# Kernel tuning notes

Measured on AMD Instinct MI355X. Metric: run time of the kernel, lower is better.

Reference implementation:

```python
import jax, jax.numpy as jnp
import numpy as np

EPS = 1e-12  # torch F.normalize default eps

def _l2norm(x):
    n = jnp.linalg.norm(x, axis=-1, keepdims=True)
    return x / jnp.maximum(n, EPS)

def setup_inputs() -> dict:
    key = jax.random.key(0)
    k1, k2, k3, k4 = jax.random.split(key, 4)
    B, D = 8192, 768           # batch, emb_d
    P, L = 4096, 8             # e_pool_size, e_p_length
    x_querry = jax.random.normal(k1, (B, D), dtype=jnp.float32)
    x_block = jax.random.normal(k2, (B, D), dtype=jnp.float32)
    # tensor_prompt uses nn.init.uniform_ -> U[0,1)
    e_k = jax.random.uniform(k3, (P, D), dtype=jnp.float32)
    e_p = jax.random.uniform(k4, (P, L, D), dtype=jnp.float32)
    return {"x_querry": x_querry, "x_block": x_block, "e_k": e_k, "e_p": e_p, "l": 3}

def reference(x_querry, x_block, e_k, e_p, l):
    # DualAdapt.forward with l=3 (e-layer), train=False: cosine-sim routing + gather
    assert l in (3, 4, 5), "reference covers the e-layer (prompt routing) path"
    n_K = _l2norm(e_k)                                  # [P, D]
    q = jax.lax.stop_gradient(_l2norm(x_querry))        # [B, D] (q is .detach()'d)
    cos_sim = jnp.einsum('bj,kj->bk', q, n_K)           # [B, P]
    k_idx = jnp.argmax(cos_sim, axis=1)                 # top_k = 1 -> indices[:, 0]
    P_ = e_p[k_idx]                                     # gather: [B, L, D]
    i = e_p.shape[1] // 2                               # e_p_length / 2
    Ek = P_[:, :i, :]                                   # [B, L/2, D]
    Ev = P_[:, i:, :]                                   # [B, L/2, D]
    # eval path: loss = 0, x_block untouched for e-layers
    return (Ek, Ev, x_block)
```

## Files before the change

kernel.cpp:

```cpp
#include <hip/hip_runtime.h>
#include <math.h>

#define NQ   8192
#define NK   4096
#define DIM  768
#define LL   8

typedef _Float16 f16;
typedef __attribute__((ext_vector_type(4))) _Float16 f16x4;
typedef __attribute__((ext_vector_type(8))) _Float16 f16x8;
typedef __attribute__((ext_vector_type(4))) float f32x4;
typedef unsigned long long u64;

__device__ inline unsigned ordf(float f) {
    unsigned u = __float_as_uint(f);
    return (u & 0x80000000u) ? ~u : (u | 0x80000000u);
}

__device__ __forceinline__ void gload16(const void* g, void* l) {
    __builtin_amdgcn_global_load_lds((const __attribute__((address_space(1))) void*)g,
                                     (__attribute__((address_space(3))) void*)l, 16, 0, 0);
}

__global__ __launch_bounds__(256) void prep(const float* __restrict__ xq,
                                            const float* __restrict__ ek,
                                            f16* __restrict__ Xh,
                                            f16* __restrict__ Eh,
                                            float* __restrict__ margin,
                                            float* __restrict__ inv_n) {
    const int wid = threadIdx.x >> 6, lane = threadIdx.x & 63;
    const int row = blockIdx.x * 4 + wid;
    const bool isX = row < NQ;
    const f32x4* src = (const f32x4*)(isX ? xq + (size_t)row * DIM
                                          : ek + (size_t)(row - NQ) * DIM);
    f16x4* dst = (f16x4*)(isX ? Xh + (size_t)row * DIM : Eh + (size_t)(row - NQ) * DIM);
    float s2 = 0.f;
#pragma unroll
    for (int j = 0; j < 3; ++j) {
        const f32x4 v = src[j * 64 + lane];
        s2 = fmaf(v.x, v.x, fmaf(v.y, v.y, fmaf(v.z, v.z, fmaf(v.w, v.w, s2))));
        dst[j * 64 + lane] = (f16x4){(f16)v.x, (f16)v.y, (f16)v.z, (f16)v.w};
    }
#pragma unroll
    for (int off = 32; off; off >>= 1) s2 += __shfl_xor(s2, off);
    if (lane == 0) {
        if (isX) margin[row] = sqrtf(s2) * 1.5e-4f + 2e-3f;
        else     inv_n[row - NQ] = 1.0f / fmaxf(sqrtf(s2), 1e-12f);
    }
}

__global__ __launch_bounds__(256) void gemm97(const f16* __restrict__ Xh,
                                              const f16* __restrict__ Eh,
                                              const float* __restrict__ inv_n,
                                              f16* __restrict__ scor) {
    __shared__ f16 A[128 * 64], B[128 * 64];
    const int t = threadIdx.x, lane = t & 63, wid = t >> 6;
    const int wm = wid & 1, wn = wid >> 1;
    const int qbase = blockIdx.x * 128, kbase = blockIdx.y * 128;

    f32x4 acc[4][4];
#pragma unroll
    for (int mi = 0; mi < 4; ++mi)
#pragma unroll
        for (int ni = 0; ni < 4; ++ni) acc[mi][ni] = (f32x4){0.f, 0.f, 0.f, 0.f};

    const int srow = wid * 8 + (lane >> 3);
    const int scol = (lane & 7) * 8;
    const f16* gA = Xh + (size_t)(qbase + srow) * DIM + scol;
    const f16* gB = Eh + (size_t)(kbase + srow) * DIM + scol;
    f16* lA = &A[wid * 512 + lane * 8];
    f16* lB = &B[wid * 512 + lane * 8];

    for (int kk = 0; kk < DIM; kk += 64) {
        __syncthreads();
#pragma unroll
        for (int p = 0; p < 4; ++p) {
            gload16(gA + (size_t)(p * 32) * DIM + kk, lA + p * 2048);
            gload16(gB + (size_t)(p * 32) * DIM + kk, lB + p * 2048);
        }
        __syncthreads();

#pragma unroll
        for (int kk2 = 0; kk2 < 2; ++kk2) {
            const int ko = kk2 * 32 + (lane >> 4) * 8;
            f16x8 ah[4], bh[4];
#pragma unroll
            for (int mi = 0; mi < 4; ++mi)
                ah[mi] = *(const f16x8*)&A[(wm * 64 + mi * 16 + (lane & 15)) * 64 + ko];
#pragma unroll
            for (int ni = 0; ni < 4; ++ni)
                bh[ni] = *(const f16x8*)&B[(wn * 64 + ni * 16 + (lane & 15)) * 64 + ko];
#pragma unroll
            for (int mi = 0; mi < 4; ++mi)
#pragma unroll
                for (int ni = 0; ni < 4; ++ni)
                    acc[mi][ni] = __builtin_amdgcn_mfma_f32_16x16x32_f16(ah[mi], bh[ni], acc[mi][ni], 0, 0, 0);
        }
    }

    const int rg = lane >> 4, cid = lane & 15;
    float invv[4];
    int key[4];
#pragma unroll
    for (int ni = 0; ni < 4; ++ni) {
        key[ni] = kbase + wn * 64 + ni * 16 + cid;
        invv[ni] = inv_n[key[ni]];
    }
#pragma unroll
    for (int mi = 0; mi < 4; ++mi)
#pragma unroll
        for (int rj = 0; rj < 4; ++rj) {
            const int row = qbase + wm * 64 + mi * 16 + rg * 4 + rj;
#pragma unroll
            for (int ni = 0; ni < 4; ++ni)
                scor[(size_t)row * NK + key[ni]] = (f16)(acc[mi][ni][rj] * invv[ni]);
        }
}

__global__ __launch_bounds__(256) void scan_rescore(const f16* __restrict__ scor,
                                                    const float* __restrict__ margin,
                                                    const float* __restrict__ inv_n,
                                                    const float* __restrict__ xq,
                                                    const float* __restrict__ ek,
                                                    int* __restrict__ bestk) {
    const int r = blockIdx.x, t = threadIdx.x, lane = t & 63, wid = t >> 6;
    __shared__ float wmaxs[4];
    __shared__ u64 wbest[4];
    __shared__ int cnt;
    __shared__ int list[256];

    if (t == 0) cnt = 0;

    const f16* srow = scor + (size_t)r * NK + t * 16;
    const f16x8 s0 = *(const f16x8*)srow;
    const f16x8 s1 = *(const f16x8*)(srow + 8);
    float sc[16];
    float m = -INFINITY;
#pragma unroll
    for (int j = 0; j < 8; ++j) { sc[j] = (float)s0[j]; sc[j + 8] = (float)s1[j]; }
#pragma unroll
    for (int j = 0; j < 16; ++j) m = fmaxf(m, sc[j]);
#pragma unroll
    for (int off = 32; off; off >>= 1) m = fmaxf(m, __shfl_xor(m, off));
    if (lane == 0) wmaxs[wid] = m;
    __syncthreads();
    m = fmaxf(fmaxf(wmaxs[0], wmaxs[1]), fmaxf(wmaxs[2], wmaxs[3]));
    const float thr = m - margin[r];

#pragma unroll
    for (int j = 0; j < 16; ++j) {
        if (sc[j] >= thr) {
            const int idx = atomicAdd(&cnt, 1);
            if (idx < 256) list[idx] = t * 16 + j;
        }
    }
    __syncthreads();
    const int n = cnt < 256 ? cnt : 256;

    const f32x4* xr = (const f32x4*)(xq + (size_t)r * DIM);
    const f32x4 xa = xr[lane * 3], xb = xr[lane * 3 + 1], xc = xr[lane * 3 + 2];

    u64 best = 0;
    for (int e = wid; e < n; e += 4) {
        const int k = list[e];
        const f32x4* er = (const f32x4*)(ek + (size_t)k * DIM);
        const f32x4 ea = er[lane * 3], eb = er[lane * 3 + 1], ec = er[lane * 3 + 2];
        float s = xa.x * ea.x;
        s = fmaf(xa.y, ea.y, s); s = fmaf(xa.z, ea.z, s); s = fmaf(xa.w, ea.w, s);
        s = fmaf(xb.x, eb.x, s); s = fmaf(xb.y, eb.y, s); s = fmaf(xb.z, eb.z, s);
        s = fmaf(xb.w, eb.w, s); s = fmaf(xc.x, ec.x, s); s = fmaf(xc.y, ec.y, s);
        s = fmaf(xc.z, ec.z, s); s = fmaf(xc.w, ec.w, s);
#pragma unroll
        for (int off = 32; off; off >>= 1) s += __shfl_xor(s, off);
        const float v = s * inv_n[k];
        const u64 p64 = ((u64)ordf(v) << 32) | (unsigned)(NK - 1 - k);
        best = best > p64 ? best : p64;
    }
    if (lane == 0) wbest[wid] = best;
    __syncthreads();
    if (t == 0) {
        u64 b0 = wbest[0];
        b0 = b0 > wbest[1] ? b0 : wbest[1];
        b0 = b0 > wbest[2] ? b0 : wbest[2];
        b0 = b0 > wbest[3] ? b0 : wbest[3];
        bestk[r] = NK - 1 - (int)(unsigned)(b0 & 0xffffffffu);
    }
}

__global__ __launch_bounds__(256) void gather_flat(const int* __restrict__ bestk,
                                                   const float* __restrict__ e_p,
                                                   const float* __restrict__ x_block,
                                                   f32x4* __restrict__ o) {
    const int EK4 = NQ * 4 * (DIM / 4);
    const int XB4 = 2 * EK4;
    const int TOT = XB4 + NQ * (DIM / 4);
    const int stride = gridDim.x * 256;
    const f32x4* ep4 = (const f32x4*)e_p;
    const f32x4* xb4 = (const f32x4*)x_block;
#pragma unroll 1
    for (int f = blockIdx.x * 256 + threadIdx.x; f < TOT; f += stride) {
        f32x4 v;
        if (f < XB4) {
            const int g = (f >= EK4) ? f - EK4 : f;
            const int b = g / (4 * DIM / 4);
            const int k = bestk[b];
            const int off = (f >= EK4) ? 4 * (DIM / 4) : 0;
            v = ep4[(size_t)k * (LL * DIM / 4) + off + (g - b * 768)];
        } else {
            v = __builtin_nontemporal_load(&xb4[f - XB4]);
        }
        __builtin_nontemporal_store(v, &o[f]);
    }
}

extern "C" void kernel_launch(void* const* d_in, const int* in_sizes, int n_in,
                              void* d_out, int out_size, void* d_ws, size_t ws_size,
                              hipStream_t stream) {
    const float* x_querry = (const float*)d_in[0];
    const float* x_block  = (const float*)d_in[1];
    const float* e_k      = (const float*)d_in[2];
    const float* e_p      = (const float*)d_in[3];

    char* base = (char*)d_out;
    f16*   Xh   = (f16*)(base);
    f16*   Eh   = (f16*)(base + 12582912);
    float* invn = (float*)(base + 18874368);
    float* marg = (float*)(base + 18890752);
    f16*   scor = (f16*)(base + 18923520);
    int*   bestk = (int*)d_ws;

    prep<<<(NQ + NK) / 4, 256, 0, stream>>>(x_querry, e_k, Xh, Eh, marg, invn);
    gemm97<<<dim3(NQ / 128, NK / 128), 256, 0, stream>>>(Xh, Eh, invn, scor);
    scan_rescore<<<NQ, 256, 0, stream>>>(scor, marg, invn, x_querry, e_k, bestk);
    gather_flat<<<2048, 256, 0, stream>>>(bestk, e_p, x_block, (f32x4*)d_out);
}
```

Baseline: 175.8 us.

## Fuse candidate filtering into GEMM epilogue, drop score matrix, enlarge tiles

```diff
diff --git a/kernel.cpp b/kernel.cpp
--- a/kernel.cpp
+++ b/kernel.cpp
@@ -5,6 +5,7 @@
 #define NK   4096
 #define DIM  768
 #define LL   8
+#define CCAP 64
 
 typedef _Float16 f16;
 typedef __attribute__((ext_vector_type(4))) _Float16 f16x4;
@@ -15,6 +16,10 @@
 __device__ inline unsigned ordf(float f) {
     unsigned u = __float_as_uint(f);
     return (u & 0x80000000u) ? ~u : (u | 0x80000000u);
+}
+__device__ inline float iord(unsigned u) {
+    unsigned b = (u & 0x80000000u) ? (u & 0x7fffffffu) : ~u;
+    return __uint_as_float(b);
 }
 
 __device__ __forceinline__ void gload16(const void* g, void* l) {
@@ -49,49 +54,50 @@
     }
 }
 
-__global__ __launch_bounds__(256) void gemm97(const f16* __restrict__ Xh,
-                                              const f16* __restrict__ Eh,
-                                              const float* __restrict__ inv_n,
-                                              f16* __restrict__ scor) {
-    __shared__ f16 A[128 * 64], B[128 * 64];
+__global__ __launch_bounds__(512, 2) void gemm256(const f16* __restrict__ Xh,
+                                                  const f16* __restrict__ Eh,
+                                                  const float* __restrict__ inv_n,
+                                                  const float* __restrict__ marg,
+                                                  int* __restrict__ cnt,
+                                                  u64* __restrict__ cand) {
+    __shared__ f16 A[256 * 64], B[256 * 64];
+    __shared__ float rmax[4][256];
     const int t = threadIdx.x, lane = t & 63, wid = t >> 6;
     const int wm = wid & 1, wn = wid >> 1;
-    const int qbase = blockIdx.x * 128, kbase = blockIdx.y * 128;
-
-    f32x4 acc[4][4];
-#pragma unroll
-    for (int mi = 0; mi < 4; ++mi)
+    const int qbase = blockIdx.x * 256, kbase = blockIdx.y * 256;
+
+    f32x4 acc[8][4];
+#pragma unroll
+    for (int mi = 0; mi < 8; ++mi)
 #pragma unroll
         for (int ni = 0; ni < 4; ++ni) acc[mi][ni] = (f32x4){0.f, 0.f, 0.f, 0.f};
 
-    const int srow = wid * 8 + (lane >> 3);
-    const int scol = (lane & 7) * 8;
-    const f16* gA = Xh + (size_t)(qbase + srow) * DIM + scol;
-    const f16* gB = Eh + (size_t)(kbase + srow) * DIM + scol;
-    f16* lA = &A[wid * 512 + lane * 8];
-    f16* lB = &B[wid * 512 + lane * 8];
+    const f16* gA = Xh + (size_t)(qbase + (t >> 3)) * DIM + (t & 7) * 8;
+    const f16* gB = Eh + (size_t)(kbase + (t >> 3)) * DIM + (t & 7) * 8;
+    f16* lA = &A[t * 8];
+    f16* lB = &B[t * 8];
 
     for (int kk = 0; kk < DIM; kk += 64) {
         __syncthreads();
 #pragma unroll
         for (int p = 0; p < 4; ++p) {
-            gload16(gA + (size_t)(p * 32) * DIM + kk, lA + p * 2048);
-            gload16(gB + (size_t)(p * 32) * DIM + kk, lB + p * 2048);
+            gload16(gA + (size_t)(p * 64) * DIM + kk, lA + p * 4096);
+            gload16(gB + (size_t)(p * 64) * DIM + kk, lB + p * 4096);
         }
         __syncthreads();
 
 #pragma unroll
         for (int kk2 = 0; kk2 < 2; ++kk2) {
             const int ko = kk2 * 32 + (lane >> 4) * 8;
-            f16x8 ah[4], bh[4];
-#pragma unroll
-            for (int mi = 0; mi < 4; ++mi)
-                ah[mi] = *(const f16x8*)&A[(wm * 64 + mi * 16 + (lane & 15)) * 64 + ko];
+            f16x8 ah[8], bh[4];
+#pragma unroll
+            for (int mi = 0; mi < 8; ++mi)
+                ah[mi] = *(const f16x8*)&A[(wm * 128 + mi * 16 + (lane & 15)) * 64 + ko];
 #pragma unroll
             for (int ni = 0; ni < 4; ++ni)
                 bh[ni] = *(const f16x8*)&B[(wn * 64 + ni * 16 + (lane & 15)) * 64 + ko];
 #pragma unroll
-            for (int mi = 0; mi < 4; ++mi)
+            for (int mi = 0; mi < 8; ++mi)
 #pragma unroll
                 for (int ni = 0; ni < 4; ++ni)
                     acc[mi][ni] = __builtin_amdgcn_mfma_f32_16x16x32_f16(ah[mi], bh[ni], acc[mi][ni], 0, 0, 0);
@@ -106,63 +112,73 @@
         key[ni] = kbase + wn * 64 + ni * 16 + cid;
         invv[ni] = inv_n[key[ni]];
     }
-#pragma unroll
-    for (int mi = 0; mi < 4; ++mi)
+
+#pragma unroll
+    for (int mi = 0; mi < 8; ++mi)
 #pragma unroll
         for (int rj = 0; rj < 4; ++rj) {
-            const int row = qbase + wm * 64 + mi * 16 + rg * 4 + rj;
-#pragma unroll
-            for (int ni = 0; ni < 4; ++ni)
-                scor[(size_t)row * NK + key[ni]] = (f16)(acc[mi][ni][rj] * invv[ni]);
-        }
-}
-
-__global__ __launch_bounds__(256) void scan_rescore(const f16* __restrict__ scor,
-                                                    const float* __restrict__ margin,
-                                                    const float* __restrict__ inv_n,
-                                                    const float* __restrict__ xq,
-                                                    const float* __restrict__ ek,
-                                                    int* __restrict__ bestk) {
-    const int r = blockIdx.x, t = threadIdx.x, lane = t & 63, wid = t >> 6;
-    __shared__ float wmaxs[4];
-    __shared__ u64 wbest[4];
-    __shared__ int cnt;
-    __shared__ int list[256];
-
-    if (t == 0) cnt = 0;
-
-    const f16* srow = scor + (size_t)r * NK + t * 16;
-    const f16x8 s0 = *(const f16x8*)srow;
-    const f16x8 s1 = *(const f16x8*)(srow + 8);
-    float sc[16];
-    float m = -INFINITY;
-#pragma unroll
-    for (int j = 0; j < 8; ++j) { sc[j] = (float)s0[j]; sc[j + 8] = (float)s1[j]; }
-#pragma unroll
-    for (int j = 0; j < 16; ++j) m = fmaxf(m, sc[j]);
-#pragma unroll
-    for (int off = 32; off; off >>= 1) m = fmaxf(m, __shfl_xor(m, off));
-    if (lane == 0) wmaxs[wid] = m;
+            float lm = acc[mi][0][rj] * invv[0];
+            lm = fmaxf(lm, acc[mi][1][rj] * invv[1]);
+            lm = fmaxf(lm, acc[mi][2][rj] * invv[2]);
+            lm = fmaxf(lm, acc[mi][3][rj] * invv[3]);
+#pragma unroll
+            for (int off = 1; off < 16; off <<= 1) lm = fmaxf(lm, __shfl_xor(lm, off));
+            if (cid == 0) rmax[wn][wm * 128 + mi * 16 + rg * 4 + rj] = lm;
+        }
     __syncthreads();
-    m = fmaxf(fmaxf(wmaxs[0], wmaxs[1]), fmaxf(wmaxs[2], wmaxs[3]));
-    const float thr = m - margin[r];
-
-#pragma unroll
-    for (int j = 0; j < 16; ++j) {
-        if (sc[j] >= thr) {
-            const int idx = atomicAdd(&cnt, 1);
-            if (idx < 256) list[idx] = t * 16 + j;
-        }
-    }
-    __syncthreads();
-    const int n = cnt < 256 ? cnt : 256;
+
+#pragma unroll
+    for (int mi = 0; mi < 8; ++mi)
+#pragma unroll
+        for (int rj = 0; rj < 4; ++rj) {
+            const int rl = wm * 128 + mi * 16 + rg * 4 + rj;
+            const float bm = fmaxf(fmaxf(rmax[0][rl], rmax[1][rl]),
+                                   fmaxf(rmax[2][rl], rmax[3][rl]));
+            const int row = qbase + rl;
+            const float thr = bm - marg[row];
+#pragma unroll
+            for (int ni = 0; ni < 4; ++ni) {
+                const float v = acc[mi][ni][rj] * invv[ni];
+                if (v >= thr) {
+                    const int idx = atomicAdd(&cnt[row], 1);
+                    if (idx < CCAP)
+                        cand[(size_t)row * CCAP + idx] =
+                            ((u64)ordf(v) << 32) | (unsigned)key[ni];
+                }
+            }
+        }
+}
+
+__global__ __launch_bounds__(256) void resolve(const int* __restrict__ cnt,
+                                               const u64* __restrict__ cand,
+                                               const float* __restrict__ marg,
+                                               const float* __restrict__ inv_n,
+                                               const float* __restrict__ xq,
+                                               const float* __restrict__ ek,
+                                               int* __restrict__ bestk) {
+    const int wid = threadIdx.x >> 6, lane = threadIdx.x & 63;
+    const int r = blockIdx.x * 4 + wid;
+    int n = cnt[r];
+    n = n < CCAP ? n : CCAP;
+    const u64* cr = cand + (size_t)r * CCAP;
+
+    u64 cm = 0;
+    for (int e = lane; e < n; e += 64) { const u64 c = cr[e]; cm = cm > c ? cm : c; }
+#pragma unroll
+    for (int off = 32; off; off >>= 1) {
+        const u64 o = __shfl_xor(cm, off);
+        cm = cm > o ? cm : o;
+    }
+    const float thr = iord((unsigned)(cm >> 32)) - marg[r];
 
     const f32x4* xr = (const f32x4*)(xq + (size_t)r * DIM);
     const f32x4 xa = xr[lane * 3], xb = xr[lane * 3 + 1], xc = xr[lane * 3 + 2];
 
     u64 best = 0;
-    for (int e = wid; e < n; e += 4) {
-        const int k = list[e];
+    for (int e = 0; e < n; ++e) {
+        const u64 c = cr[e];
+        if (iord((unsigned)(c >> 32)) < thr) continue;
+        const int k = (int)(unsigned)(c & 0xffffffffu);
         const f32x4* er = (const f32x4*)(ek + (size_t)k * DIM);
         const f32x4 ea = er[lane * 3], eb = er[lane * 3 + 1], ec = er[lane * 3 + 2];
         float s = xa.x * ea.x;
@@ -172,19 +188,11 @@
         s = fmaf(xc.z, ec.z, s); s = fmaf(xc.w, ec.w, s);
 #pragma unroll
         for (int off = 32; off; off >>= 1) s += __shfl_xor(s, off);
-        const float v = s * inv_n[k];
-        const u64 p64 = ((u64)ordf(v) << 32) | (unsigned)(NK - 1 - k);
+        const float ve = s * inv_n[k];
+        const u64 p64 = ((u64)ordf(ve) << 32) | (unsigned)(NK - 1 - k);
         best = best > p64 ? best : p64;
     }
-    if (lane == 0) wbest[wid] = best;
-    __syncthreads();
-    if (t == 0) {
-        u64 b0 = wbest[0];
-        b0 = b0 > wbest[1] ? b0 : wbest[1];
-        b0 = b0 > wbest[2] ? b0 : wbest[2];
-        b0 = b0 > wbest[3] ? b0 : wbest[3];
-        bestk[r] = NK - 1 - (int)(unsigned)(b0 & 0xffffffffu);
-    }
+    if (lane == 0) bestk[r] = NK - 1 - (int)(unsigned)(best & 0xffffffffu);
 }
 
 __global__ __launch_bounds__(256) void gather_flat(const int* __restrict__ bestk,
@@ -226,11 +234,13 @@
     f16*   Eh   = (f16*)(base + 12582912);
     float* invn = (float*)(base + 18874368);
     float* marg = (float*)(base + 18890752);
-    f16*   scor = (f16*)(base + 18923520);
+    int*   cnt  = (int*)(base + 18923520);
+    u64*   cand = (u64*)(base + 18956288);
     int*   bestk = (int*)d_ws;
 
+    hipMemsetAsync(cnt, 0, NQ * sizeof(int), stream);
     prep<<<(NQ + NK) / 4, 256, 0, stream>>>(x_querry, e_k, Xh, Eh, marg, invn);
-    gemm97<<<dim3(NQ / 128, NK / 128), 256, 0, stream>>>(Xh, Eh, invn, scor);
-    scan_rescore<<<NQ, 256, 0, stream>>>(scor, marg, invn, x_querry, e_k, bestk);
+    gemm256<<<dim3(NQ / 256, NK / 256), 512, 0, stream>>>(Xh, Eh, invn, marg, cnt, cand);
+    resolve<<<NQ / 4, 256, 0, stream>>>(cnt, cand, marg, invn, x_querry, e_k, bestk);
     gather_flat<<<2048, 256, 0, stream>>>(bestk, e_p, x_block, (f32x4*)d_out);
 }
```

Result: slower. 225.4 us (+28.2%).

## Use 256x256 double-buffered GEMM tile with XOR-swizzled LDS and setprio

Applied to the files above, without the earlier changes.

```diff
diff --git a/kernel.cpp b/kernel.cpp
--- a/kernel.cpp
+++ b/kernel.cpp
@@ -49,54 +49,89 @@
     }
 }
 
-__global__ __launch_bounds__(256) void gemm97(const f16* __restrict__ Xh,
-                                              const f16* __restrict__ Eh,
-                                              const float* __restrict__ inv_n,
-                                              f16* __restrict__ scor) {
-    __shared__ f16 A[128 * 64], B[128 * 64];
+__global__ __launch_bounds__(512, 2) void gemm256p(const f16* __restrict__ Xh,
+                                                   const f16* __restrict__ Eh,
+                                                   const float* __restrict__ inv_n,
+                                                   f16* __restrict__ scor) {
+    __shared__ f16 A[2][256 * 64], B[2][256 * 64];
     const int t = threadIdx.x, lane = t & 63, wid = t >> 6;
     const int wm = wid & 1, wn = wid >> 1;
-    const int qbase = blockIdx.x * 128, kbase = blockIdx.y * 128;
-
-    f32x4 acc[4][4];
-#pragma unroll
-    for (int mi = 0; mi < 4; ++mi)
+    const int qbase = blockIdx.x * 256, kbase = blockIdx.y * 256;
+
+    f32x4 acc[8][4];
+#pragma unroll
+    for (int mi = 0; mi < 8; ++mi)
 #pragma unroll
         for (int ni = 0; ni < 4; ++ni) acc[mi][ni] = (f32x4){0.f, 0.f, 0.f, 0.f};
 
-    const int srow = wid * 8 + (lane >> 3);
-    const int scol = (lane & 7) * 8;
-    const f16* gA = Xh + (size_t)(qbase + srow) * DIM + scol;
-    const f16* gB = Eh + (size_t)(kbase + srow) * DIM + scol;
-    f16* lA = &A[wid * 512 + lane * 8];
-    f16* lB = &B[wid * 512 + lane * 8];
-
-    for (int kk = 0; kk < DIM; kk += 64) {
-        __syncthreads();
-#pragma unroll
-        for (int p = 0; p < 4; ++p) {
-            gload16(gA + (size_t)(p * 32) * DIM + kk, lA + p * 2048);
-            gload16(gB + (size_t)(p * 32) * DIM + kk, lB + p * 2048);
-        }
-        __syncthreads();
-
-#pragma unroll
-        for (int kk2 = 0; kk2 < 2; ++kk2) {
-            const int ko = kk2 * 32 + (lane >> 4) * 8;
-            f16x8 ah[4], bh[4];
-#pragma unroll
-            for (int mi = 0; mi < 4; ++mi)
-                ah[mi] = *(const f16x8*)&A[(wm * 64 + mi * 16 + (lane & 15)) * 64 + ko];
-#pragma unroll
-            for (int ni = 0; ni < 4; ++ni)
-                bh[ni] = *(const f16x8*)&B[(wn * 64 + ni * 16 + (lane & 15)) * 64 + ko];
-#pragma unroll
-            for (int mi = 0; mi < 4; ++mi)
-#pragma unroll
-                for (int ni = 0; ni < 4; ++ni)
-                    acc[mi][ni] = __builtin_amdgcn_mfma_f32_16x16x32_f16(ah[mi], bh[ni], acc[mi][ni], 0, 0, 0);
-        }
-    }
+    const int srow = t >> 3, sslot = t & 7;
+    const int gslot = sslot ^ (srow & 7);
+    const f16* gA = Xh + (size_t)(qbase + srow) * DIM + gslot * 8;
+    const f16* gB = Eh + (size_t)(kbase + srow) * DIM + gslot * 8;
+
+#define STAGE(buf, kk)                                                        \
+    {                                                                         \
+        _Pragma("unroll")                                                     \
+        for (int p = 0; p < 4; ++p) {                                         \
+            gload16(gA + (size_t)(p * 64) * DIM + (kk), &A[buf][p * 4096 + t * 8]); \
+            gload16(gB + (size_t)(p * 64) * DIM + (kk), &B[buf][p * 4096 + t * 8]); \
+        }                                                                     \
+    }
+
+    const int rlow = lane & 15, quad = lane >> 4;
+
+#define TILE_COMPUTE(cur)                                                     \
+    {                                                                         \
+        _Pragma("unroll")                                                     \
+        for (int kk2 = 0; kk2 < 2; ++kk2) {                                   \
+            f16x8 bh[4];                                                      \
+            _Pragma("unroll")                                                 \
+            for (int ni = 0; ni < 4; ++ni) {                                  \
+                const int r = wn * 64 + ni * 16 + rlow;                       \
+                const int s = (kk2 * 4 + quad) ^ (r & 7);                     \
+                bh[ni] = *(const f16x8*)&B[cur][r * 64 + s * 8];              \
+            }                                                                 \
+            _Pragma("unroll")                                                 \
+            for (int h = 0; h < 2; ++h) {                                     \
+                f16x8 ah[4];                                                  \
+                _Pragma("unroll")                                             \
+                for (int i = 0; i < 4; ++i) {                                 \
+                    const int r = wm * 128 + (h * 4 + i) * 16 + rlow;         \
+                    const int s = (kk2 * 4 + quad) ^ (r & 7);                 \
+                    ah[i] = *(const f16x8*)&A[cur][r * 64 + s * 8];           \
+                }                                                             \
+                __builtin_amdgcn_s_setprio(1);                                \
+                _Pragma("unroll")                                             \
+                for (int i = 0; i < 4; ++i)                                   \
+                    _Pragma("unroll")                                         \
+                    for (int ni = 0; ni < 4; ++ni)                            \
+                        acc[h * 4 + i][ni] = __builtin_amdgcn_mfma_f32_16x16x32_f16( \
+                            ah[i], bh[ni], acc[h * 4 + i][ni], 0, 0, 0);      \
+                __builtin_amdgcn_s_setprio(0);                                \
+            }                                                                 \
+        }                                                                     \
+    }
+
+    STAGE(0, 0);
+
+#pragma unroll 1
+    for (int tt = 0; tt < 11; ++tt) {
+        const int cur = tt & 1;
+        STAGE(cur ^ 1, (tt + 1) * 64);
+        asm volatile("s_waitcnt vmcnt(8)" ::: "memory");
+        __builtin_amdgcn_sched_barrier(0);
+        __builtin_amdgcn_s_barrier();
+        __builtin_amdgcn_sched_barrier(0);
+        if (cur) TILE_COMPUTE(1) else TILE_COMPUTE(0);
+        __builtin_amdgcn_sched_barrier(0);
+        __builtin_amdgcn_s_barrier();
+        __builtin_amdgcn_sched_barrier(0);
+    }
+    asm volatile("s_waitcnt vmcnt(0)" ::: "memory");
+    __builtin_amdgcn_sched_barrier(0);
+    __builtin_amdgcn_s_barrier();
+    __builtin_amdgcn_sched_barrier(0);
+    TILE_COMPUTE(1);
 
     const int rg = lane >> 4, cid = lane & 15;
     float invv[4];
@@ -107,14 +142,16 @@
         invv[ni] = inv_n[key[ni]];
     }
 #pragma unroll
-    for (int mi = 0; mi < 4; ++mi)
+    for (int mi = 0; mi < 8; ++mi)
 #pragma unroll
         for (int rj = 0; rj < 4; ++rj) {
-            const int row = qbase + wm * 64 + mi * 16 + rg * 4 + rj;
+            const int row = qbase + wm * 128 + mi * 16 + rg * 4 + rj;
 #pragma unroll
             for (int ni = 0; ni < 4; ++ni)
                 scor[(size_t)row * NK + key[ni]] = (f16)(acc[mi][ni][rj] * invv[ni]);
         }
+#undef STAGE
+#undef TILE_COMPUTE
 }
 
 __global__ __launch_bounds__(256) void scan_rescore(const f16* __restrict__ scor,
@@ -230,7 +267,7 @@
     int*   bestk = (int*)d_ws;
 
     prep<<<(NQ + NK) / 4, 256, 0, stream>>>(x_querry, e_k, Xh, Eh, marg, invn);
-    gemm97<<<dim3(NQ / 128, NK / 128), 256, 0, stream>>>(Xh, Eh, invn, scor);
+    gemm256p<<<dim3(NQ / 256, NK / 256), 512, 0, stream>>>(Xh, Eh, invn, scor);
     scan_rescore<<<NQ, 256, 0, stream>>>(scor, marg, invn, x_querry, e_k, bestk);
     gather_flat<<<2048, 256, 0, stream>>>(bestk, e_p, x_block, (f32x4*)d_out);
 }
```

Measured after the change: 343.9 us. 1.96x slower.

## Rewrite GEMM as 256x256 tile with 8 waves, LDS double-buffering and swizzle

Applied to the files above, without the earlier changes.

```diff
diff --git a/kernel.cpp b/kernel.cpp
--- a/kernel.cpp
+++ b/kernel.cpp
@@ -49,53 +49,85 @@
     }
 }
 
-__global__ __launch_bounds__(256) void gemm97(const f16* __restrict__ Xh,
-                                              const f16* __restrict__ Eh,
-                                              const float* __restrict__ inv_n,
-                                              f16* __restrict__ scor) {
-    __shared__ f16 A[128 * 64], B[128 * 64];
+__global__ __launch_bounds__(512, 2) void gemm8p(const f16* __restrict__ Xh,
+                                                 const f16* __restrict__ Eh,
+                                                 const float* __restrict__ inv_n,
+                                                 f16* __restrict__ scor) {
+    __shared__ f16 Al[2][256 * 64], Bl[2][256 * 64];
     const int t = threadIdx.x, lane = t & 63, wid = t >> 6;
     const int wm = wid & 1, wn = wid >> 1;
-    const int qbase = blockIdx.x * 128, kbase = blockIdx.y * 128;
-
-    f32x4 acc[4][4];
-#pragma unroll
-    for (int mi = 0; mi < 4; ++mi)
+    const int qbase = blockIdx.x * 256, kbase = blockIdx.y * 256;
+
+    f32x4 acc[8][4];
+#pragma unroll
+    for (int mi = 0; mi < 8; ++mi)
 #pragma unroll
         for (int ni = 0; ni < 4; ++ni) acc[mi][ni] = (f32x4){0.f, 0.f, 0.f, 0.f};
 
-    const int srow = wid * 8 + (lane >> 3);
-    const int scol = (lane & 7) * 8;
-    const f16* gA = Xh + (size_t)(qbase + srow) * DIM + scol;
-    const f16* gB = Eh + (size_t)(kbase + srow) * DIM + scol;
-    f16* lA = &A[wid * 512 + lane * 8];
-    f16* lB = &B[wid * 512 + lane * 8];
-
-    for (int kk = 0; kk < DIM; kk += 64) {
+    const int srow = t >> 3;
+    const int gslot = (t & 7) ^ (srow & 7);
+    const f16* gA = Xh + (size_t)(qbase + srow) * DIM + gslot * 8;
+    const f16* gB = Eh + (size_t)(kbase + srow) * DIM + gslot * 8;
+
+#pragma unroll
+    for (int p = 0; p < 4; ++p) {
+        gload16(gA + (size_t)(p * 64) * DIM, &Al[0][p * 4096 + t * 8]);
+        gload16(gB + (size_t)(p * 64) * DIM, &Bl[0][p * 4096 + t * 8]);
+    }
+    __syncthreads();
+
+    const int rlow = lane & 15, quad = lane >> 4;
+
+#pragma unroll 1
+    for (int tt = 0; tt < 12; ++tt) {
+        const int cur = tt & 1;
+        const f16* Ab = Al[cur];
+        const f16* Bb = Bl[cur];
+        f16* An = Al[cur ^ 1];
+        f16* Bn = Bl[cur ^ 1];
+        const bool pf = (tt + 1) < 12;
+        const size_t knext = (size_t)(tt + 1) * 64;
+
+        f16x8 bh[4][2];
+#pragma unroll
+        for (int p = 0; p < 4; ++p) {
+            if (p == 0) {
+#pragma unroll
+                for (int ni = 0; ni < 4; ++ni)
+#pragma unroll
+                    for (int k2 = 0; k2 < 2; ++k2) {
+                        const int r = wn * 64 + ni * 16 + rlow;
+                        const int s = (k2 * 4 + quad) ^ (r & 7);
+                        bh[ni][k2] = *(const f16x8*)&Bb[r * 64 + s * 8];
+                    }
+            }
+            f16x8 ah[2][2];
+#pragma unroll
+            for (int q = 0; q < 2; ++q)
+#pragma unroll
+                for (int k2 = 0; k2 < 2; ++k2) {
+                    const int r = wm * 128 + (p * 2 + q) * 16 + rlow;
+                    const int s = (k2 * 4 + quad) ^ (r & 7);
+                    ah[q][k2] = *(const f16x8*)&Ab[r * 64 + s * 8];
+                }
+            if (pf) {
+                gload16(gA + (size_t)(p * 64) * DIM + knext, &An[p * 4096 + t * 8]);
+                gload16(gB + (size_t)(p * 64) * DIM + knext, &Bn[p * 4096 + t * 8]);
+            }
+            __builtin_amdgcn_s_barrier();
+            __builtin_amdgcn_s_setprio(1);
+#pragma unroll
+            for (int q = 0; q < 2; ++q)
+#pragma unroll
+                for (int k2 = 0; k2 < 2; ++k2)
+#pragma unroll
+                    for (int ni = 0; ni < 4; ++ni)
+                        acc[p * 2 + q][ni] = __builtin_amdgcn_mfma_f32_16x16x32_f16(
+                            ah[q][k2], bh[ni][k2], acc[p * 2 + q][ni], 0, 0, 0);
+            __builtin_amdgcn_s_setprio(0);
+            if (p < 3) __builtin_amdgcn_s_barrier();
+        }
         __syncthreads();
-#pragma unroll
-        for (int p = 0; p < 4; ++p) {
-            gload16(gA + (size_t)(p * 32) * DIM + kk, lA + p * 2048);
-            gload16(gB + (size_t)(p * 32) * DIM + kk, lB + p * 2048);
-        }
-        __syncthreads();
-
-#pragma unroll
-        for (int kk2 = 0; kk2 < 2; ++kk2) {
-            const int ko = kk2 * 32 + (lane >> 4) * 8;
-            f16x8 ah[4], bh[4];
-#pragma unroll
-            for (int mi = 0; mi < 4; ++mi)
-                ah[mi] = *(const f16x8*)&A[(wm * 64 + mi * 16 + (lane & 15)) * 64 + ko];
-#pragma unroll
-            for (int ni = 0; ni < 4; ++ni)
-                bh[ni] = *(const f16x8*)&B[(wn * 64 + ni * 16 + (lane & 15)) * 64 + ko];
-#pragma unroll
-            for (int mi = 0; mi < 4; ++mi)
-#pragma unroll
-                for (int ni = 0; ni < 4; ++ni)
-                    acc[mi][ni] = __builtin_amdgcn_mfma_f32_16x16x32_f16(ah[mi], bh[ni], acc[mi][ni], 0, 0, 0);
-        }
     }
 
     const int rg = lane >> 4, cid = lane & 15;
@@ -107,10 +139,10 @@
         invv[ni] = inv_n[key[ni]];
     }
 #pragma unroll
-    for (int mi = 0; mi < 4; ++mi)
+    for (int mi = 0; mi < 8; ++mi)
 #pragma unroll
         for (int rj = 0; rj < 4; ++rj) {
-            const int row = qbase + wm * 64 + mi * 16 + rg * 4 + rj;
+            const int row = qbase + wm * 128 + mi * 16 + rg * 4 + rj;
 #pragma unroll
             for (int ni = 0; ni < 4; ++ni)
                 scor[(size_t)row * NK + key[ni]] = (f16)(acc[mi][ni][rj] * invv[ni]);
@@ -230,7 +262,7 @@
     int*   bestk = (int*)d_ws;
 
     prep<<<(NQ + NK) / 4, 256, 0, stream>>>(x_querry, e_k, Xh, Eh, marg, invn);
-    gemm97<<<dim3(NQ / 128, NK / 128), 256, 0, stream>>>(Xh, Eh, invn, scor);
+    gemm8p<<<dim3(NQ / 256, NK / 256), 512, 0, stream>>>(Xh, Eh, invn, scor);
     scan_rescore<<<NQ, 256, 0, stream>>>(scor, marg, invn, x_querry, e_k, bestk);
     gather_flat<<<2048, 256, 0, stream>>>(bestk, e_p, x_block, (f32x4*)d_out);
 }
```

Measured after the change: 151.6 us. 1.16x faster.
